# Performance work log

Measured on AMD Instinct MI355X. Metric: run time of the kernel, lower is better.

The kernel has to match this reference:

```python
import jax, jax.numpy as jnp
import numpy as np

NEMB = 128
N_NODES = 8192
N_EDGES = 16384
N_STEMS = 4096
N_GRAPHS = 256
N_BLOCKS = 105       # BlockDictionary.n_unique_blocks
N_STEMTYPES = 32     # BlockDictionary.n_stem_types
OUT_PER_STEM = 105
OUT_PER_STOP = 1
NUM_CONV_STEPS = 12
SLOPE = 0.01         # nn.LeakyReLU default negative slope


def _act(v):
    return jax.nn.leaky_relu(v, SLOPE)


def setup_inputs() -> dict:
    key = jax.random.key(0)
    ks = jax.random.split(key, 32)
    def p(i, shape, fan_in):
        return jax.random.normal(ks[i], shape, jnp.float32) / np.sqrt(fan_in).astype(np.float32)
    D = NEMB
    inp = {
        "x": jax.random.randint(ks[0], (N_NODES,), 0, N_BLOCKS + 1),
        "stemtypes": jax.random.randint(ks[1], (N_STEMS,), 0, N_STEMTYPES + 1),
        "edge_attr": jax.random.randint(ks[2], (N_EDGES, 2), 0, N_STEMTYPES),
        "edge_index": jax.random.randint(ks[3], (2, N_EDGES), 0, N_NODES),
        "stem_node_idx": jax.random.randint(ks[4], (N_STEMS,), 0, N_NODES),
        "node_batch": jnp.sort(jax.random.randint(ks[5], (N_NODES,), 0, N_GRAPHS)),
        # embedding tables
        "emb_block": p(6, (N_BLOCKS + 1, D), D),
        "emb_stem": p(7, (N_STEMTYPES + 1, D), D),
        "emb_bond": p(8, (N_STEMTYPES, D), D),
        # block2emb MLP
        "b2e_w1": p(9, (D, D), D), "b2e_b1": p(10, (D,), D),
        "b2e_w2": p(11, (D, D), D), "b2e_b2": p(12, (D,), D),
        # NNConv root weight + bias (edge-nn is identity: nn.Sequential())
        "conv_root": p(13, (D, D), D), "conv_bias": p(14, (D,), D),
        # GRU (torch gate order r, z, n)
        "gru_w_ih": p(15, (3 * D, D), D), "gru_w_hh": p(16, (3 * D, D), D),
        "gru_b_ih": p(17, (3 * D,), D), "gru_b_hh": p(18, (3 * D,), D),
        # stem2pred MLP (in = 2*D)
        "s2p_w1": p(19, (D, 2 * D), 2 * D), "s2p_b1": p(20, (D,), 2 * D),
        "s2p_w2": p(21, (D, D), D), "s2p_b2": p(22, (D,), D),
        "s2p_w3": p(23, (OUT_PER_STEM, D), D), "s2p_b3": p(24, (OUT_PER_STEM,), D),
        # global2pred MLP
        "g2p_w1": p(25, (D, D), D), "g2p_b1": p(26, (D,), D),
        "g2p_w2": p(27, (OUT_PER_STOP, D), D), "g2p_b2": p(28, (OUT_PER_STOP,), D),
    }
    return inp


def reference(x, stemtypes, edge_attr, edge_index, stem_node_idx, node_batch,
              emb_block, emb_stem, emb_bond,
              b2e_w1, b2e_b1, b2e_w2, b2e_b2,
              conv_root, conv_bias,
              gru_w_ih, gru_w_hh, gru_b_ih, gru_b_hh,
              s2p_w1, s2p_b1, s2p_w2, s2p_b2, s2p_w3, s2p_b3,
              g2p_w1, g2p_b1, g2p_w2, g2p_b2):
    block_emb = emb_block[x]                          # [N, D]
    stem_emb = emb_stem[stemtypes]                    # [S, D]
    be = emb_bond[edge_attr]                          # [E, 2, D]
    # outer product -> per-edge [D_in, D_out] weight (matches view(-1, in, out))
    W_e = be[:, 0, :, None] * be[:, 1, None, :]       # [E, D, D]

    out = _act(block_emb @ b2e_w1.T + b2e_b1) @ b2e_w2.T + b2e_b2  # [N, D]
    h = out                                           # GRU hidden state

    src, dst = edge_index[0], edge_index[1]
    ones_e = jnp.ones((N_EDGES,), out.dtype)
    deg = jax.ops.segment_sum(ones_e, dst, num_segments=N_NODES)
    inv_deg = jnp.where(deg > 0, 1.0 / jnp.maximum(deg, 1.0), 0.0)[:, None]

    for _ in range(NUM_CONV_STEPS):
        # NNConv: mean_j (x_j @ W_e) + x @ root + bias, then LeakyReLU
        msg = jnp.einsum('ei,eij->ej', out[src], W_e)                  # [E, D]
        agg = jax.ops.segment_sum(msg, dst, num_segments=N_NODES) * inv_deg
        m = _act(agg + out @ conv_root + conv_bias)
        # single-layer GRU, seq_len = 1
        gi = m @ gru_w_ih.T + gru_b_ih
        gh = h @ gru_w_hh.T + gru_b_hh
        ir, iz, inn = jnp.split(gi, 3, axis=-1)
        hr, hz, hn = jnp.split(gh, 3, axis=-1)
        r = jax.nn.sigmoid(ir + hr)
        z = jax.nn.sigmoid(iz + hz)
        n = jnp.tanh(inn + r * hn)
        h = (1.0 - z) * n + z * h
        out = h

    stem_cat = jnp.concatenate([out[stem_node_idx], stem_emb], axis=1)  # [S, 2D]
    s = _act(stem_cat @ s2p_w1.T + s2p_b1)
    s = _act(s @ s2p_w2.T + s2p_b2)
    stem_pred = s @ s2p_w3.T + s2p_b3                                   # [S, out_per_stem]

    # global_mean_pool
    gsum = jax.ops.segment_sum(out, node_batch, num_segments=N_GRAPHS)
    gcnt = jax.ops.segment_sum(jnp.ones((N_NODES,), out.dtype), node_batch, num_segments=N_GRAPHS)
    gmean = gsum / jnp.maximum(gcnt, 1.0)[:, None]
    g = _act(gmean @ g2p_w1.T + g2p_b1)
    stop_pred = g @ g2p_w2.T + g2p_b2                                   # [G, out_per_stop]
    return stem_pred, stop_pred
```

## Files before the change

### kernel.cpp

```cpp
#include <hip/hip_runtime.h>
#include <math.h>

#define D 128
#define NNODES 8192
#define NEDGES 16384
#define NSTEMS 4096
#define NGRAPHS 256
#define NSTEPS 12
#define OPS 105
#define SLOPE 0.01f
#define MT 32
#define NB (NNODES / MT)
#define LDA 136
#define LDA2 264
#define LDQ 40
#define LDH 132

typedef _Float16 half_t;
typedef __attribute__((ext_vector_type(8))) _Float16 f16x8;
typedef __attribute__((ext_vector_type(4))) float f32x4;

__device__ __forceinline__ float leaky(float x) { return x > 0.f ? x : SLOPE * x; }
__device__ __forceinline__ float fast_sigmoid(float x) {
    return __builtin_amdgcn_rcpf(1.f + __expf(-x));
}
__device__ __forceinline__ float fast_tanh(float x) {
    float e = __expf(2.f * x);
    return 1.f - 2.f * __builtin_amdgcn_rcpf(e + 1.f);
}

__global__ void k_setup(
    const float* __restrict__ root, const float* __restrict__ wih,
    const float* __restrict__ whh, const float* __restrict__ bond,
    const float* __restrict__ sw1, const float* __restrict__ sw2,
    const float* __restrict__ sw3, const float* __restrict__ bw1,
    const float* __restrict__ bw2, const float* __restrict__ gw1,
    half_t* __restrict__ rootP, half_t* __restrict__ WihP,
    half_t* __restrict__ WhhP, half_t* __restrict__ bondTP,
    half_t* __restrict__ s1P, half_t* __restrict__ s2P, half_t* __restrict__ s3P,
    half_t* __restrict__ w1P, half_t* __restrict__ w2P, half_t* __restrict__ bondQP,
    float* __restrict__ g1T, int* __restrict__ zeroi) {
    int idx = blockIdx.x * 256 + threadIdx.x;
    int which = blockIdx.y;
    if (which == 10) {
        if (idx < 128 * 128) {
            int r = idx >> 7, c = idx & 127;
            g1T[c * 128 + r] = gw1[idx];
        }
        return;
    }
    if (which == 11) {
        if (idx < 2 * NNODES) zeroi[idx] = 0;
        return;
    }
    int KT = (which == 4) ? 8 : (which == 9) ? 1 : 4;
    int NT = (which == 1 || which == 2) ? 24 : (which == 3) ? 2 : (which == 6) ? 7 : 8;
    if (idx >= NT * KT * 512) return;
    int j = idx & 7;
    int L = (idx >> 3) & 63;
    int t = idx >> 9;
    int kt = t % KT, nt = t / KT;
    int k = kt * 32 + (L >> 4) * 8 + j;
    int n = nt * 16 + (L & 15);
    switch (which) {
        case 0: rootP[idx] = (half_t)root[k * D + n]; break;
        case 1: WihP[idx] = (half_t)wih[n * D + k]; break;
        case 2: WhhP[idx] = (half_t)whh[n * D + k]; break;
        case 3: bondTP[idx] = (half_t)bond[n * D + k]; break;
        case 4: s1P[idx] = (half_t)sw1[n * 256 + k]; break;
        case 5: s2P[idx] = (half_t)sw2[n * 128 + k]; break;
        case 6: s3P[idx] = (n < OPS) ? (half_t)sw3[n * 128 + k] : (half_t)0.f; break;
        case 7: w1P[idx] = (half_t)bw1[n * D + k]; break;
        case 8: w2P[idx] = (half_t)bw2[n * D + k]; break;
        case 9: bondQP[idx] = (half_t)bond[k * D + n]; break;
    }
}

__global__ void k_deg(const int* __restrict__ eidx, int* __restrict__ deg) {
    int e = blockIdx.x * 256 + threadIdx.x;
    if (e < NEDGES) atomicAdd(&deg[eidx[NEDGES + e]], 1);
}

__global__ void k_scan(const int* __restrict__ deg, int* __restrict__ row_start,
                       float* __restrict__ inv_deg) {
    __shared__ int sums[256];
    int t = threadIdx.x;
    int base = t * 32;
    int s = 0;
    for (int k = 0; k < 32; ++k) s += deg[base + k];
    sums[t] = s;
    __syncthreads();
    for (int off = 1; off < 256; off <<= 1) {
        int v = sums[t];
        int u = (t >= off) ? sums[t - off] : 0;
        __syncthreads();
        sums[t] = v + u;
        __syncthreads();
    }
    int run = sums[t] - s;
    for (int k = 0; k < 32; ++k) {
        int d = deg[base + k];
        row_start[base + k] = run;
        run += d;
        inv_deg[base + k] = (d > 0) ? (1.0f / (float)d) : 0.0f;
    }
    if (t == 255) row_start[NNODES] = run;
}

__global__ void k_scatter(const int* __restrict__ eidx, const int* __restrict__ eattr,
                          const int* __restrict__ row_start,
                          int* __restrict__ fill, int4* __restrict__ epack) {
    int e = blockIdx.x * 256 + threadIdx.x;
    if (e < NEDGES) {
        int d = eidx[NEDGES + e];
        int pos = row_start[d] + atomicAdd(&fill[d], 1);
        int2 aa = *(const int2*)(eattr + 2 * e);
        epack[pos] = make_int4(eidx[e], aa.x, aa.y, d);
    }
}

__global__ __launch_bounds__(512, 2) void k_init(
    const int* __restrict__ x, const float* __restrict__ embBlock,
    const half_t* __restrict__ w1P, const float* __restrict__ b1,
    const half_t* __restrict__ w2P, const float* __restrict__ b2,
    const half_t* __restrict__ bondTP,
    float* __restrict__ hF, float* __restrict__ P0) {
    __shared__ __align__(16) half_t Ae[MT * LDA];
    __shared__ __align__(16) half_t T1[MT * LDA];
    const int tid = threadIdx.x;
    const int w = tid >> 6;
    const int lane = tid & 63;
    const int quad = lane >> 4;
    const int l16 = lane & 15;
    const int n0 = blockIdx.x * MT;
    const int c = w * 16 + l16;

    {
        int row = tid >> 4;
        int col = (tid & 15) * 8;
        const float* src = embBlock + (size_t)x[n0 + row] * D + col;
        float4 v0 = ((const float4*)src)[0];
        float4 v1 = ((const float4*)src)[1];
        f16x8 hv;
        hv[0] = (half_t)v0.x; hv[1] = (half_t)v0.y; hv[2] = (half_t)v0.z; hv[3] = (half_t)v0.w;
        hv[4] = (half_t)v1.x; hv[5] = (half_t)v1.y; hv[6] = (half_t)v1.z; hv[7] = (half_t)v1.w;
        *(f16x8*)&Ae[row * LDA + col] = hv;
    }
    __syncthreads();

    {
        f32x4 acc[2] = {{0.f, 0.f, 0.f, 0.f}, {0.f, 0.f, 0.f, 0.f}};
#pragma unroll
        for (int kt = 0; kt < 4; ++kt) {
            f16x8 b = *(const f16x8*)(w1P + (size_t)((w * 4 + kt) * 64 + lane) * 8);
            f16x8 a0 = *(const f16x8*)&Ae[(0 + l16) * LDA + kt * 32 + quad * 8];
            f16x8 a1 = *(const f16x8*)&Ae[(16 + l16) * LDA + kt * 32 + quad * 8];
            acc[0] = __builtin_amdgcn_mfma_f32_16x16x32_f16(a0, b, acc[0], 0, 0, 0);
            acc[1] = __builtin_amdgcn_mfma_f32_16x16x32_f16(a1, b, acc[1], 0, 0, 0);
        }
        float bb = b1[c];
#pragma unroll
        for (int mt = 0; mt < 2; ++mt)
#pragma unroll
            for (int r = 0; r < 4; ++r)
                T1[(mt * 16 + quad * 4 + r) * LDA + c] = (half_t)leaky(acc[mt][r] + bb);
    }
    __syncthreads();

    {
        f32x4 acc[2] = {{0.f, 0.f, 0.f, 0.f}, {0.f, 0.f, 0.f, 0.f}};
#pragma unroll
        for (int kt = 0; kt < 4; ++kt) {
            f16x8 b = *(const f16x8*)(w2P + (size_t)((w * 4 + kt) * 64 + lane) * 8);
            f16x8 a0 = *(const f16x8*)&T1[(0 + l16) * LDA + kt * 32 + quad * 8];
            f16x8 a1 = *(const f16x8*)&T1[(16 + l16) * LDA + kt * 32 + quad * 8];
            acc[0] = __builtin_amdgcn_mfma_f32_16x16x32_f16(a0, b, acc[0], 0, 0, 0);
            acc[1] = __builtin_amdgcn_mfma_f32_16x16x32_f16(a1, b, acc[1], 0, 0, 0);
        }
        float bb = b2[c];
#pragma unroll
        for (int mt = 0; mt < 2; ++mt)
#pragma unroll
            for (int r = 0; r < 4; ++r) {
                int row = mt * 16 + quad * 4 + r;
                float h = acc[mt][r] + bb;
                hF[(size_t)(n0 + row) * D + c] = h;
                Ae[row * LDA + c] = (half_t)h;
            }
    }
    __syncthreads();

    if (w < 4) {
        int mt = w >> 1, nt = w & 1;
        f32x4 acc = {0.f, 0.f, 0.f, 0.f};
#pragma unroll
        for (int kt = 0; kt < 4; ++kt) {
            f16x8 b = *(const f16x8*)(bondTP + (size_t)((nt * 4 + kt) * 64 + lane) * 8);
            f16x8 a = *(const f16x8*)&Ae[(mt * 16 + l16) * LDA + kt * 32 + quad * 8];
            acc = __builtin_amdgcn_mfma_f32_16x16x32_f16(a, b, acc, 0, 0, 0);
        }
#pragma unroll
        for (int r = 0; r < 4; ++r)
            P0[(size_t)(n0 + mt * 16 + quad * 4 + r) * 32 + nt * 16 + l16] = acc[r];
    }
}

__global__ __launch_bounds__(512, 2) void k_step(
    float* __restrict__ hF,
    const float* __restrict__ Pprev, float* __restrict__ Pnext,
    const half_t* __restrict__ rootP, const half_t* __restrict__ WihP,
    const half_t* __restrict__ WhhP, const half_t* __restrict__ bondTP,
    const half_t* __restrict__ bondQP,
    const float* __restrict__ cbias, const float* __restrict__ bih,
    const float* __restrict__ bhh,
    const int4* __restrict__ epack,
    const int* __restrict__ row_start, const float* __restrict__ inv_deg, int writeP) {
    __shared__ __align__(16) half_t As[MT * LDA];
    __shared__ __align__(16) half_t Am[MT * LDA];
    __shared__ __align__(16) float Hs[MT * LDH];
    __shared__ __align__(16) half_t Qh[MT * LDQ];
    __shared__ float Q[MT * 32];

    const int tid = threadIdx.x;
    const int w = tid >> 6;
    const int lane = tid & 63;
    const int quad = lane >> 4;
    const int l16 = lane & 15;
    const int n0 = blockIdx.x * MT;
    const int c = w * 16 + l16;

    {
        int row = tid >> 4;
        int col = (tid & 15) * 8;
        const float* src = hF + (size_t)(n0 + row) * D + col;
        float4 v0 = ((const float4*)src)[0];
        float4 v1 = ((const float4*)src)[1];
        f16x8 hv;
        hv[0] = (half_t)v0.x; hv[1] = (half_t)v0.y; hv[2] = (half_t)v0.z; hv[3] = (half_t)v0.w;
        hv[4] = (half_t)v1.x; hv[5] = (half_t)v1.y; hv[6] = (half_t)v1.z; hv[7] = (half_t)v1.w;
        *(f16x8*)&As[row * LDA + col] = hv;
        *(float4*)&Hs[row * LDH + col] = v0;
        *(float4*)&Hs[row * LDH + col + 4] = v1;
    }
    Q[tid] = 0.f;
    Q[tid + 512] = 0.f;
    const int p0 = row_start[n0];
    const int p1 = row_start[n0 + MT];
    int4 ep;
    float wv = 0.f, idg = 0.f;
    const int pme = p0 + tid;
    const bool have = (pme < p1);
    if (have) {
        ep = epack[pme];
        wv = Pprev[(size_t)ep.x * 32 + ep.y];
        idg = inv_deg[ep.w];
    }
    f16x8 rootB[4], ghB[12], aggB;
#pragma unroll
    for (int kt = 0; kt < 4; ++kt)
        rootB[kt] = *(const f16x8*)(rootP + (size_t)((w * 4 + kt) * 64 + lane) * 8);
#pragma unroll
    for (int kt = 0; kt < 4; ++kt)
#pragma unroll
        for (int g = 0; g < 3; ++g)
            ghB[g * 4 + kt] = *(const f16x8*)(WhhP + (size_t)(((g * 8 + w) * 4 + kt) * 64 + lane) * 8);
    aggB = *(const f16x8*)(bondQP + (size_t)(w * 64 + lane) * 8);
    const float cb = cbias[c];
    const float bi0 = bih[c], bi1 = bih[D + c], bi2 = bih[2 * D + c];
    const float bh0 = bhh[c], bh1 = bhh[D + c], bh2 = bhh[2 * D + c];
    __syncthreads();

    f32x4 convAcc[2] = {{0.f, 0.f, 0.f, 0.f}, {0.f, 0.f, 0.f, 0.f}};
#pragma unroll
    for (int kt = 0; kt < 4; ++kt) {
        f16x8 a0 = *(const f16x8*)&As[(0 + l16) * LDA + kt * 32 + quad * 8];
        f16x8 a1 = *(const f16x8*)&As[(16 + l16) * LDA + kt * 32 + quad * 8];
        convAcc[0] = __builtin_amdgcn_mfma_f32_16x16x32_f16(a0, rootB[kt], convAcc[0], 0, 0, 0);
        convAcc[1] = __builtin_amdgcn_mfma_f32_16x16x32_f16(a1, rootB[kt], convAcc[1], 0, 0, 0);
    }
    if (have) atomicAdd(&Q[(ep.w - n0) * 32 + ep.z], wv * idg);
    for (int p2 = pme + 512; p2 < p1; p2 += 512) {
        int4 e2 = epack[p2];
        atomicAdd(&Q[(e2.w - n0) * 32 + e2.z], Pprev[(size_t)e2.x * 32 + e2.y] * inv_deg[e2.w]);
    }
    f32x4 ghA[2][3];
#pragma unroll
    for (int mt = 0; mt < 2; ++mt)
#pragma unroll
        for (int g = 0; g < 3; ++g) ghA[mt][g] = f32x4{0.f, 0.f, 0.f, 0.f};
#pragma unroll
    for (int kt = 0; kt < 4; ++kt) {
        f16x8 a0 = *(const f16x8*)&As[(0 + l16) * LDA + kt * 32 + quad * 8];
        f16x8 a1 = *(const f16x8*)&As[(16 + l16) * LDA + kt * 32 + quad * 8];
#pragma unroll
        for (int g = 0; g < 3; ++g) {
            ghA[0][g] = __builtin_amdgcn_mfma_f32_16x16x32_f16(a0, ghB[g * 4 + kt], ghA[0][g], 0, 0, 0);
            ghA[1][g] = __builtin_amdgcn_mfma_f32_16x16x32_f16(a1, ghB[g * 4 + kt], ghA[1][g], 0, 0, 0);
        }
    }
    __syncthreads();

    f16x8 giB[12];
#pragma unroll
    for (int kt = 0; kt < 4; ++kt)
#pragma unroll
        for (int g = 0; g < 3; ++g)
            giB[g * 4 + kt] = *(const f16x8*)(WihP + (size_t)(((g * 8 + w) * 4 + kt) * 64 + lane) * 8);

    Qh[(tid >> 5) * LDQ + (tid & 31)] = (half_t)Q[tid];
    Qh[((tid + 512) >> 5) * LDQ + (tid & 31)] = (half_t)Q[tid + 512];
    __syncthreads();

#pragma unroll
    for (int mt = 0; mt < 2; ++mt) {
        f32x4 acc = {0.f, 0.f, 0.f, 0.f};
        f16x8 a = *(const f16x8*)&Qh[(mt * 16 + l16) * LDQ + quad * 8];
        acc = __builtin_amdgcn_mfma_f32_16x16x32_f16(a, aggB, acc, 0, 0, 0);
#pragma unroll
        for (int r = 0; r < 4; ++r) {
            float m = convAcc[mt][r] + cb + acc[r];
            Am[(mt * 16 + quad * 4 + r) * LDA + c] = (half_t)leaky(m);
        }
    }
    __syncthreads();

    f32x4 giA[2][3];
#pragma unroll
    for (int mt = 0; mt < 2; ++mt)
#pragma unroll
        for (int g = 0; g < 3; ++g) giA[mt][g] = f32x4{0.f, 0.f, 0.f, 0.f};
#pragma unroll
    for (int kt = 0; kt < 4; ++kt) {
        f16x8 a0 = *(const f16x8*)&Am[(0 + l16) * LDA + kt * 32 + quad * 8];
        f16x8 a1 = *(const f16x8*)&Am[(16 + l16) * LDA + kt * 32 + quad * 8];
#pragma unroll
        for (int g = 0; g < 3; ++g) {
            giA[0][g] = __builtin_amdgcn_mfma_f32_16x16x32_f16(a0, giB[g * 4 + kt], giA[0][g], 0, 0, 0);
            giA[1][g] = __builtin_amdgcn_mfma_f32_16x16x32_f16(a1, giB[g * 4 + kt], giA[1][g], 0, 0, 0);
        }
    }
#pragma unroll
    for (int mt = 0; mt < 2; ++mt) {
#pragma unroll
        for (int r = 0; r < 4; ++r) {
            int row = mt * 16 + quad * 4 + r;
            float rg = fast_sigmoid(giA[mt][0][r] + bi0 + ghA[mt][0][r] + bh0);
            float z = fast_sigmoid(giA[mt][1][r] + bi1 + ghA[mt][1][r] + bh1);
            float nn = fast_tanh(giA[mt][2][r] + bi2 + rg * (ghA[mt][2][r] + bh2));
            float hnew = (1.f - z) * nn + z * Hs[row * LDH + c];
            hF[(size_t)(n0 + row) * D + c] = hnew;
            As[row * LDA + c] = (half_t)hnew;
        }
    }

    if (writeP) {
        __syncthreads();
        if (w < 4) {
            int mt = w >> 1, nt = w & 1;
            f32x4 acc = {0.f, 0.f, 0.f, 0.f};
#pragma unroll
            for (int kt = 0; kt < 4; ++kt) {
                f16x8 b = *(const f16x8*)(bondTP + (size_t)((nt * 4 + kt) * 64 + lane) * 8);
                f16x8 a = *(const f16x8*)&As[(mt * 16 + l16) * LDA + kt * 32 + quad * 8];
                acc = __builtin_amdgcn_mfma_f32_16x16x32_f16(a, b, acc, 0, 0, 0);
            }
#pragma unroll
            for (int r = 0; r < 4; ++r)
                Pnext[(size_t)(n0 + mt * 16 + quad * 4 + r) * 32 + nt * 16 + l16] = acc[r];
        }
    }
}

__device__ __forceinline__ int lower_bound_dev(const int* a, int n, int v) {
    int lo = 0, hi = n;
    while (lo < hi) {
        int m = (lo + hi) >> 1;
        if (a[m] < v) lo = m + 1;
        else hi = m;
    }
    return lo;
}

__global__ __launch_bounds__(512) void k_heads(
    const float* __restrict__ hF, const int* __restrict__ sni, const int* __restrict__ stypes,
    const float* __restrict__ embStem,
    const half_t* __restrict__ s1P, const float* __restrict__ b1,
    const half_t* __restrict__ s2P, const float* __restrict__ b2,
    const half_t* __restrict__ s3P, const float* __restrict__ b3,
    const int* __restrict__ batch,
    const float* __restrict__ g1T, const float* __restrict__ gb1,
    const float* __restrict__ gw2, const float* __restrict__ gb2,
    float* __restrict__ dout) {
    __shared__ __align__(16) half_t cat[16 * LDA2];
    __shared__ __align__(16) half_t t1[16 * LDA];
    __shared__ __align__(16) half_t t2[16 * LDA];
    const int tid = threadIdx.x;
    if (blockIdx.x >= 256) {
        int g = blockIdx.x - 256;
        if (tid >= 128) return;
        __shared__ float mean_s[D];
        __shared__ float red[D];
        int j = tid;
        int lo = lower_bound_dev(batch, NNODES, g);
        int hi = lower_bound_dev(batch, NNODES, g + 1);
        float sum = 0.f;
        for (int n = lo; n < hi; ++n) sum += hF[(size_t)n * D + j];
        float denom = (hi > lo) ? (float)(hi - lo) : 1.0f;
        mean_s[j] = sum / denom;
        __syncthreads();
        float a = gb1[j];
        for (int i = 0; i < D; ++i) a += mean_s[i] * g1T[i * D + j];
        a = leaky(a);
        red[j] = a * gw2[j];
        __syncthreads();
        for (int off = 64; off > 0; off >>= 1) {
            if (j < off) red[j] += red[j + off];
            __syncthreads();
        }
        if (j == 0) dout[NSTEMS * OPS + g] = red[0] + gb2[0];
        return;
    }
    const int w = tid >> 6;
    const int lane = tid & 63;
    const int quad = lane >> 4;
    const int l16 = lane & 15;
    const int s0 = blockIdx.x * 16;
    const int c = w * 16 + l16;

    {
        int row = tid >> 5;
        int col = (tid & 31) * 8;
        const float* src;
        if (col < D) src = hF + (size_t)sni[s0 + row] * D + col;
        else src = embStem + (size_t)stypes[s0 + row] * D + (col - D);
        float4 v0 = ((const float4*)src)[0];
        float4 v1 = ((const float4*)src)[1];
        f16x8 hv;
        hv[0] = (half_t)v0.x; hv[1] = (half_t)v0.y; hv[2] = (half_t)v0.z; hv[3] = (half_t)v0.w;
        hv[4] = (half_t)v1.x; hv[5] = (half_t)v1.y; hv[6] = (half_t)v1.z; hv[7] = (half_t)v1.w;
        *(f16x8*)&cat[row * LDA2 + col] = hv;
    }
    __syncthreads();

    {
        f32x4 acc = {0.f, 0.f, 0.f, 0.f};
#pragma unroll
        for (int kt = 0; kt < 8; ++kt) {
            f16x8 b = *(const f16x8*)(s1P + (size_t)((w * 8 + kt) * 64 + lane) * 8);
            f16x8 a = *(const f16x8*)&cat[l16 * LDA2 + kt * 32 + quad * 8];
            acc = __builtin_amdgcn_mfma_f32_16x16x32_f16(a, b, acc, 0, 0, 0);
        }
        float bb = b1[c];
#pragma unroll
        for (int r = 0; r < 4; ++r)
            t1[(quad * 4 + r) * LDA + c] = (half_t)leaky(acc[r] + bb);
    }
    __syncthreads();
    {
        f32x4 acc = {0.f, 0.f, 0.f, 0.f};
#pragma unroll
        for (int kt = 0; kt < 4; ++kt) {
            f16x8 b = *(const f16x8*)(s2P + (size_t)((w * 4 + kt) * 64 + lane) * 8);
            f16x8 a = *(const f16x8*)&t1[l16 * LDA + kt * 32 + quad * 8];
            acc = __builtin_amdgcn_mfma_f32_16x16x32_f16(a, b, acc, 0, 0, 0);
        }
        float bb = b2[c];
#pragma unroll
        for (int r = 0; r < 4; ++r)
            t2[(quad * 4 + r) * LDA + c] = (half_t)leaky(acc[r] + bb);
    }
    __syncthreads();
    if (w < 7) {
        f32x4 acc = {0.f, 0.f, 0.f, 0.f};
#pragma unroll
        for (int kt = 0; kt < 4; ++kt) {
            f16x8 b = *(const f16x8*)(s3P + (size_t)((w * 4 + kt) * 64 + lane) * 8);
            f16x8 a = *(const f16x8*)&t2[l16 * LDA + kt * 32 + quad * 8];
            acc = __builtin_amdgcn_mfma_f32_16x16x32_f16(a, b, acc, 0, 0, 0);
        }
        int j = w * 16 + l16;
        if (j < OPS) {
            float bb = b3[j];
#pragma unroll
            for (int r = 0; r < 4; ++r)
                dout[(size_t)(s0 + quad * 4 + r) * OPS + j] = acc[r] + bb;
        }
    }
}

extern "C" void kernel_launch(void* const* d_in, const int* in_sizes, int n_in,
                              void* d_out, int out_size, void* d_ws, size_t ws_size,
                              hipStream_t stream) {
    const int* x = (const int*)d_in[0];
    const int* stypes = (const int*)d_in[1];
    const int* eattr = (const int*)d_in[2];
    const int* eidx = (const int*)d_in[3];
    const int* sni = (const int*)d_in[4];
    const int* batch = (const int*)d_in[5];
    const float* embBlock = (const float*)d_in[6];
    const float* embStem = (const float*)d_in[7];
    const float* embBond = (const float*)d_in[8];
    const float* b2e_w1 = (const float*)d_in[9];
    const float* b2e_b1 = (const float*)d_in[10];
    const float* b2e_w2 = (const float*)d_in[11];
    const float* b2e_b2 = (const float*)d_in[12];
    const float* conv_root = (const float*)d_in[13];
    const float* conv_bias = (const float*)d_in[14];
    const float* gru_w_ih = (const float*)d_in[15];
    const float* gru_w_hh = (const float*)d_in[16];
    const float* gru_b_ih = (const float*)d_in[17];
    const float* gru_b_hh = (const float*)d_in[18];
    const float* s2p_w1 = (const float*)d_in[19];
    const float* s2p_b1 = (const float*)d_in[20];
    const float* s2p_w2 = (const float*)d_in[21];
    const float* s2p_b2 = (const float*)d_in[22];
    const float* s2p_w3 = (const float*)d_in[23];
    const float* s2p_b3 = (const float*)d_in[24];
    const float* g2p_w1 = (const float*)d_in[25];
    const float* g2p_b1 = (const float*)d_in[26];
    const float* g2p_w2 = (const float*)d_in[27];
    const float* g2p_b2 = (const float*)d_in[28];
    float* out_f = (float*)d_out;

    float* W = (float*)d_ws;
    size_t off = 0;
    auto alloc = [&](size_t words) {
        size_t o = off;
        off += (words + 3) & ~(size_t)3;
        return o;
    };
    float* hF = W + alloc(NNODES * D);
    float* P0 = W + alloc(NNODES * 32);
    float* P1 = W + alloc(NNODES * 32);
    half_t* rootP = (half_t*)(W + alloc(16384 / 2));
    half_t* WihP = (half_t*)(W + alloc(49152 / 2));
    half_t* WhhP = (half_t*)(W + alloc(49152 / 2));
    half_t* bondTP = (half_t*)(W + alloc(4096 / 2));
    half_t* s1P = (half_t*)(W + alloc(32768 / 2));
    half_t* s2P = (half_t*)(W + alloc(16384 / 2));
    half_t* s3P = (half_t*)(W + alloc(14336 / 2));
    half_t* w1P = (half_t*)(W + alloc(16384 / 2));
    half_t* w2P = (half_t*)(W + alloc(16384 / 2));
    half_t* bondQP = (half_t*)(W + alloc(4096 / 2));
    float* g1T = W + alloc(128 * 128);
    int* row_start = (int*)(W + alloc(NNODES + 1));
    int4* epack = (int4*)(W + alloc(NEDGES * 4));
    float* inv_deg = W + alloc(NNODES);
    float* zbase = W + alloc(2 * NNODES);
    int* deg = (int*)zbase;
    int* fill = deg + NNODES;

    k_setup<<<dim3(192, 12), 256, 0, stream>>>(
        conv_root, gru_w_ih, gru_w_hh, embBond, s2p_w1, s2p_w2, s2p_w3,
        b2e_w1, b2e_w2, g2p_w1,
        rootP, WihP, WhhP, bondTP, s1P, s2P, s3P, w1P, w2P, bondQP,
        g1T, (int*)zbase);
    k_deg<<<(NEDGES + 255) / 256, 256, 0, stream>>>(eidx, deg);
    k_scan<<<1, 256, 0, stream>>>(deg, row_start, inv_deg);
    k_scatter<<<(NEDGES + 255) / 256, 256, 0, stream>>>(eidx, eattr, row_start, fill, epack);
    k_init<<<NNODES / MT, 512, 0, stream>>>(x, embBlock, w1P, b2e_b1, w2P, b2e_b2,
                                            bondTP, hF, P0);

    for (int step = 0; step < NSTEPS; ++step) {
        const float* Pprev = (step & 1) ? P1 : P0;
        float* Pnext = (step & 1) ? P0 : P1;
        int writeP = (step < NSTEPS - 1) ? 1 : 0;
        k_step<<<NB, 512, 0, stream>>>(
            hF, Pprev, Pnext, rootP, WihP, WhhP, bondTP, bondQP,
            conv_bias, gru_b_ih, gru_b_hh,
            epack, row_start, inv_deg, writeP);
    }

    k_heads<<<NSTEMS / 16 + NGRAPHS, 512, 0, stream>>>(
        hF, sni, stypes, embStem,
        s1P, s2p_b1, s2P, s2p_b2, s3P, s2p_b3,
        batch, g1T, g2p_b1, g2p_w2, g2p_b2, out_f);
}
```

Baseline: 251.7 us.

## Use 64-node tiles with 1024-thread blocks in GRU step kernel

The step kernel now processes 64 nodes per block with 16 waves: each column-wave pair splits the rows in two halves, so each weight fragment is shared across twice as many rows per block and the grid is halved. The old h values are read straight from global memory into registers rather than staged in a shared fp32 buffer. The weight fragments are also loaded inside the MFMA loops instead of being preloaded into registers, which lowers register pressure enough for 1024-thread blocks. In exchange there are fewer blocks (128) on a large GPU, which may underfill the compute units, and global weight loads now sit inside the MFMA loops where they can stall.

```diff
diff --git a/kernel.cpp b/kernel.cpp
--- a/kernel.cpp
+++ b/kernel.cpp
@@ -9,12 +9,12 @@
 #define NSTEPS 12
 #define OPS 105
 #define SLOPE 0.01f
-#define MT 32
-#define NB (NNODES / MT)
+#define IMT 32
+#define SMT 64
+#define NSB (NNODES / SMT)
 #define LDA 136
 #define LDA2 264
 #define LDQ 40
-#define LDH 132
 
 typedef _Float16 half_t;
 typedef __attribute__((ext_vector_type(8))) _Float16 f16x8;
@@ -125,14 +125,14 @@
     const half_t* __restrict__ w2P, const float* __restrict__ b2,
     const half_t* __restrict__ bondTP,
     float* __restrict__ hF, float* __restrict__ P0) {
-    __shared__ __align__(16) half_t Ae[MT * LDA];
-    __shared__ __align__(16) half_t T1[MT * LDA];
+    __shared__ __align__(16) half_t Ae[IMT * LDA];
+    __shared__ __align__(16) half_t T1[IMT * LDA];
     const int tid = threadIdx.x;
     const int w = tid >> 6;
     const int lane = tid & 63;
     const int quad = lane >> 4;
     const int l16 = lane & 15;
-    const int n0 = blockIdx.x * MT;
+    const int n0 = blockIdx.x * IMT;
     const int c = w * 16 + l16;
 
     {
@@ -205,7 +205,7 @@
     }
 }
 
-__global__ __launch_bounds__(512, 2) void k_step(
+__global__ __launch_bounds__(1024, 1) void k_step(
     float* __restrict__ hF,
     const float* __restrict__ Pprev, float* __restrict__ Pnext,
     const half_t* __restrict__ rootP, const half_t* __restrict__ WihP,
@@ -215,19 +215,20 @@
     const float* __restrict__ bhh,
     const int4* __restrict__ epack,
     const int* __restrict__ row_start, const float* __restrict__ inv_deg, int writeP) {
-    __shared__ __align__(16) half_t As[MT * LDA];
-    __shared__ __align__(16) half_t Am[MT * LDA];
-    __shared__ __align__(16) float Hs[MT * LDH];
-    __shared__ __align__(16) half_t Qh[MT * LDQ];
-    __shared__ float Q[MT * 32];
+    __shared__ __align__(16) half_t As[SMT * LDA];
+    __shared__ __align__(16) half_t Am[SMT * LDA];
+    __shared__ __align__(16) half_t Qh[SMT * LDQ];
+    __shared__ float Q[SMT * 32];
 
     const int tid = threadIdx.x;
     const int w = tid >> 6;
     const int lane = tid & 63;
     const int quad = lane >> 4;
     const int l16 = lane & 15;
-    const int n0 = blockIdx.x * MT;
-    const int c = w * 16 + l16;
+    const int wc = w & 7;
+    const int mh = w >> 3;
+    const int n0 = blockIdx.x * SMT;
+    const int c = wc * 16 + l16;
 
     {
         int row = tid >> 4;
@@ -239,13 +240,17 @@
         hv[0] = (half_t)v0.x; hv[1] = (half_t)v0.y; hv[2] = (half_t)v0.z; hv[3] = (half_t)v0.w;
         hv[4] = (half_t)v1.x; hv[5] = (half_t)v1.y; hv[6] = (half_t)v1.z; hv[7] = (half_t)v1.w;
         *(f16x8*)&As[row * LDA + col] = hv;
-        *(float4*)&Hs[row * LDH + col] = v0;
-        *(float4*)&Hs[row * LDH + col + 4] = v1;
-    }
+    }
+    float hold[2][4];
+#pragma unroll
+    for (int mt = 0; mt < 2; ++mt)
+#pragma unroll
+        for (int r = 0; r < 4; ++r)
+            hold[mt][r] = hF[(size_t)(n0 + (mh * 2 + mt) * 16 + quad * 4 + r) * D + c];
     Q[tid] = 0.f;
-    Q[tid + 512] = 0.f;
+    Q[tid + 1024] = 0.f;
     const int p0 = row_start[n0];
-    const int p1 = row_start[n0 + MT];
+    const int p1 = row_start[n0 + SMT];
     int4 ep;
     float wv = 0.f, idg = 0.f;
     const int pme = p0 + tid;
@@ -255,16 +260,7 @@
         wv = Pprev[(size_t)ep.x * 32 + ep.y];
         idg = inv_deg[ep.w];
     }
-    f16x8 rootB[4], ghB[12], aggB;
-#pragma unroll
-    for (int kt = 0; kt < 4; ++kt)
-        rootB[kt] = *(const f16x8*)(rootP + (size_t)((w * 4 + kt) * 64 + lane) * 8);
-#pragma unroll
-    for (int kt = 0; kt < 4; ++kt)
-#pragma unroll
-        for (int g = 0; g < 3; ++g)
-            ghB[g * 4 + kt] = *(const f16x8*)(WhhP + (size_t)(((g * 8 + w) * 4 + kt) * 64 + lane) * 8);
-    aggB = *(const f16x8*)(bondQP + (size_t)(w * 64 + lane) * 8);
+    f16x8 aggB = *(const f16x8*)(bondQP + (size_t)(wc * 64 + lane) * 8);
     const float cb = cbias[c];
     const float bi0 = bih[c], bi1 = bih[D + c], bi2 = bih[2 * D + c];
     const float bh0 = bhh[c], bh1 = bhh[D + c], bh2 = bhh[2 * D + c];
@@ -273,13 +269,14 @@
     f32x4 convAcc[2] = {{0.f, 0.f, 0.f, 0.f}, {0.f, 0.f, 0.f, 0.f}};
 #pragma unroll
     for (int kt = 0; kt < 4; ++kt) {
-        f16x8 a0 = *(const f16x8*)&As[(0 + l16) * LDA + kt * 32 + quad * 8];
-        f16x8 a1 = *(const f16x8*)&As[(16 + l16) * LDA + kt * 32 + quad * 8];
-        convAcc[0] = __builtin_amdgcn_mfma_f32_16x16x32_f16(a0, rootB[kt], convAcc[0], 0, 0, 0);
-        convAcc[1] = __builtin_amdgcn_mfma_f32_16x16x32_f16(a1, rootB[kt], convAcc[1], 0, 0, 0);
+        f16x8 b = *(const f16x8*)(rootP + (size_t)((wc * 4 + kt) * 64 + lane) * 8);
+        f16x8 a0 = *(const f16x8*)&As[((mh * 2 + 0) * 16 + l16) * LDA + kt * 32 + quad * 8];
+        f16x8 a1 = *(const f16x8*)&As[((mh * 2 + 1) * 16 + l16) * LDA + kt * 32 + quad * 8];
+        convAcc[0] = __builtin_amdgcn_mfma_f32_16x16x32_f16(a0, b, convAcc[0], 0, 0, 0);
+        convAcc[1] = __builtin_amdgcn_mfma_f32_16x16x32_f16(a1, b, convAcc[1], 0, 0, 0);
     }
     if (have) atomicAdd(&Q[(ep.w - n0) * 32 + ep.z], wv * idg);
-    for (int p2 = pme + 512; p2 < p1; p2 += 512) {
+    for (int p2 = pme + 1024; p2 < p1; p2 += 1024) {
         int4 e2 = epack[p2];
         atomicAdd(&Q[(e2.w - n0) * 32 + e2.z], Pprev[(size_t)e2.x * 32 + e2.y] * inv_deg[e2.w]);
     }
@@ -290,36 +287,30 @@
         for (int g = 0; g < 3; ++g) ghA[mt][g] = f32x4{0.f, 0.f, 0.f, 0.f};
 #pragma unroll
     for (int kt = 0; kt < 4; ++kt) {
-        f16x8 a0 = *(const f16x8*)&As[(0 + l16) * LDA + kt * 32 + quad * 8];
-        f16x8 a1 = *(const f16x8*)&As[(16 + l16) * LDA + kt * 32 + quad * 8];
+        f16x8 a0 = *(const f16x8*)&As[((mh * 2 + 0) * 16 + l16) * LDA + kt * 32 + quad * 8];
+        f16x8 a1 = *(const f16x8*)&As[((mh * 2 + 1) * 16 + l16) * LDA + kt * 32 + quad * 8];
 #pragma unroll
         for (int g = 0; g < 3; ++g) {
-            ghA[0][g] = __builtin_amdgcn_mfma_f32_16x16x32_f16(a0, ghB[g * 4 + kt], ghA[0][g], 0, 0, 0);
-            ghA[1][g] = __builtin_amdgcn_mfma_f32_16x16x32_f16(a1, ghB[g * 4 + kt], ghA[1][g], 0, 0, 0);
-        }
-    }
-    __syncthreads();
-
-    f16x8 giB[12];
-#pragma unroll
-    for (int kt = 0; kt < 4; ++kt)
-#pragma unroll
-        for (int g = 0; g < 3; ++g)
-            giB[g * 4 + kt] = *(const f16x8*)(WihP + (size_t)(((g * 8 + w) * 4 + kt) * 64 + lane) * 8);
+            f16x8 b = *(const f16x8*)(WhhP + (size_t)(((g * 8 + wc) * 4 + kt) * 64 + lane) * 8);
+            ghA[0][g] = __builtin_amdgcn_mfma_f32_16x16x32_f16(a0, b, ghA[0][g], 0, 0, 0);
+            ghA[1][g] = __builtin_amdgcn_mfma_f32_16x16x32_f16(a1, b, ghA[1][g], 0, 0, 0);
+        }
+    }
+    __syncthreads();
 
     Qh[(tid >> 5) * LDQ + (tid & 31)] = (half_t)Q[tid];
-    Qh[((tid + 512) >> 5) * LDQ + (tid & 31)] = (half_t)Q[tid + 512];
+    Qh[((tid + 1024) >> 5) * LDQ + (tid & 31)] = (half_t)Q[tid + 1024];
     __syncthreads();
 
 #pragma unroll
     for (int mt = 0; mt < 2; ++mt) {
         f32x4 acc = {0.f, 0.f, 0.f, 0.f};
-        f16x8 a = *(const f16x8*)&Qh[(mt * 16 + l16) * LDQ + quad * 8];
+        f16x8 a = *(const f16x8*)&Qh[((mh * 2 + mt) * 16 + l16) * LDQ + quad * 8];
         acc = __builtin_amdgcn_mfma_f32_16x16x32_f16(a, aggB, acc, 0, 0, 0);
 #pragma unroll
         for (int r = 0; r < 4; ++r) {
             float m = convAcc[mt][r] + cb + acc[r];
-            Am[(mt * 16 + quad * 4 + r) * LDA + c] = (half_t)leaky(m);
+            Am[((mh * 2 + mt) * 16 + quad * 4 + r) * LDA + c] = (half_t)leaky(m);
         }
     }
     __syncthreads();
@@ -331,23 +322,24 @@
         for (int g = 0; g < 3; ++g) giA[mt][g] = f32x4{0.f, 0.f, 0.f, 0.f};
 #pragma unroll
     for (int kt = 0; kt < 4; ++kt) {
-        f16x8 a0 = *(const f16x8*)&Am[(0 + l16) * LDA + kt * 32 + quad * 8];
-        f16x8 a1 = *(const f16x8*)&Am[(16 + l16) * LDA + kt * 32 + quad * 8];
+        f16x8 a0 = *(const f16x8*)&Am[((mh * 2 + 0) * 16 + l16) * LDA + kt * 32 + quad * 8];
+        f16x8 a1 = *(const f16x8*)&Am[((mh * 2 + 1) * 16 + l16) * LDA + kt * 32 + quad * 8];
 #pragma unroll
         for (int g = 0; g < 3; ++g) {
-            giA[0][g] = __builtin_amdgcn_mfma_f32_16x16x32_f16(a0, giB[g * 4 + kt], giA[0][g], 0, 0, 0);
-            giA[1][g] = __builtin_amdgcn_mfma_f32_16x16x32_f16(a1, giB[g * 4 + kt], giA[1][g], 0, 0, 0);
+            f16x8 b = *(const f16x8*)(WihP + (size_t)(((g * 8 + wc) * 4 + kt) * 64 + lane) * 8);
+            giA[0][g] = __builtin_amdgcn_mfma_f32_16x16x32_f16(a0, b, giA[0][g], 0, 0, 0);
+            giA[1][g] = __builtin_amdgcn_mfma_f32_16x16x32_f16(a1, b, giA[1][g], 0, 0, 0);
         }
     }
 #pragma unroll
     for (int mt = 0; mt < 2; ++mt) {
 #pragma unroll
         for (int r = 0; r < 4; ++r) {
-            int row = mt * 16 + quad * 4 + r;
+            int row = (mh * 2 + mt) * 16 + quad * 4 + r;
             float rg = fast_sigmoid(giA[mt][0][r] + bi0 + ghA[mt][0][r] + bh0);
             float z = fast_sigmoid(giA[mt][1][r] + bi1 + ghA[mt][1][r] + bh1);
             float nn = fast_tanh(giA[mt][2][r] + bi2 + rg * (ghA[mt][2][r] + bh2));
-            float hnew = (1.f - z) * nn + z * Hs[row * LDH + c];
+            float hnew = (1.f - z) * nn + z * hold[mt][r];
             hF[(size_t)(n0 + row) * D + c] = hnew;
             As[row * LDA + c] = (half_t)hnew;
         }
@@ -355,7 +347,7 @@
 
     if (writeP) {
         __syncthreads();
-        if (w < 4) {
+        if (w < 8) {
             int mt = w >> 1, nt = w & 1;
             f32x4 acc = {0.f, 0.f, 0.f, 0.f};
 #pragma unroll
@@ -558,14 +550,14 @@
     k_deg<<<(NEDGES + 255) / 256, 256, 0, stream>>>(eidx, deg);
     k_scan<<<1, 256, 0, stream>>>(deg, row_start, inv_deg);
     k_scatter<<<(NEDGES + 255) / 256, 256, 0, stream>>>(eidx, eattr, row_start, fill, epack);
-    k_init<<<NNODES / MT, 512, 0, stream>>>(x, embBlock, w1P, b2e_b1, w2P, b2e_b2,
-                                            bondTP, hF, P0);
+    k_init<<<NNODES / IMT, 512, 0, stream>>>(x, embBlock, w1P, b2e_b1, w2P, b2e_b2,
+                                             bondTP, hF, P0);
 
     for (int step = 0; step < NSTEPS; ++step) {
         const float* Pprev = (step & 1) ? P1 : P0;
         float* Pnext = (step & 1) ? P0 : P1;
         int writeP = (step < NSTEPS - 1) ? 1 : 0;
-        k_step<<<NB, 512, 0, stream>>>(
+        k_step<<<NSB, 1024, 0, stream>>>(
             hF, Pprev, Pnext, rootP, WihP, WhhP, bondTP, bondQP,
             conv_bias, gru_b_ih, gru_b_hh,
             epack, row_start, inv_deg, writeP);
```

After: 283.4 us. +12.6%, slower.

## Store GRU hidden state in fp16 ping-pong buffers and fuse CSR build

Applied to the files above, without the earlier changes.

Hidden state between GRU steps is now kept as fp16 in two ping-pong buffers instead of fp32. This halves the per-step state traffic and removes the fp32 shared-memory copy of h. Only the last step writes fp32 output. The degree count, scan and scatter kernels are merged into one single-block kernel using shared-memory atomics, which removes two launches and the zeroing pass. The cost is lower precision in the recurrent state and a serial single-block CSR build.

```diff
diff --git a/kernel.cpp b/kernel.cpp
--- a/kernel.cpp
+++ b/kernel.cpp
@@ -14,7 +14,6 @@
 #define LDA 136
 #define LDA2 264
 #define LDQ 40
-#define LDH 132
 
 typedef _Float16 half_t;
 typedef __attribute__((ext_vector_type(8))) _Float16 f16x8;
@@ -39,7 +38,7 @@
     half_t* __restrict__ WhhP, half_t* __restrict__ bondTP,
     half_t* __restrict__ s1P, half_t* __restrict__ s2P, half_t* __restrict__ s3P,
     half_t* __restrict__ w1P, half_t* __restrict__ w2P, half_t* __restrict__ bondQP,
-    float* __restrict__ g1T, int* __restrict__ zeroi) {
+    float* __restrict__ g1T) {
     int idx = blockIdx.x * 256 + threadIdx.x;
     int which = blockIdx.y;
     if (which == 10) {
@@ -47,10 +46,6 @@
             int r = idx >> 7, c = idx & 127;
             g1T[c * 128 + r] = gw1[idx];
         }
-        return;
-    }
-    if (which == 11) {
-        if (idx < 2 * NNODES) zeroi[idx] = 0;
         return;
     }
     int KT = (which == 4) ? 8 : (which == 9) ? 1 : 4;
@@ -76,44 +71,45 @@
     }
 }
 
-__global__ void k_deg(const int* __restrict__ eidx, int* __restrict__ deg) {
-    int e = blockIdx.x * 256 + threadIdx.x;
-    if (e < NEDGES) atomicAdd(&deg[eidx[NEDGES + e]], 1);
-}
-
-__global__ void k_scan(const int* __restrict__ deg, int* __restrict__ row_start,
-                       float* __restrict__ inv_deg) {
-    __shared__ int sums[256];
-    int t = threadIdx.x;
-    int base = t * 32;
+__global__ __launch_bounds__(1024) void k_csr(
+    const int* __restrict__ eidx, const int* __restrict__ eattr,
+    int* __restrict__ row_start, float* __restrict__ inv_deg,
+    int4* __restrict__ epack) {
+    __shared__ int sdeg[NNODES];
+    __shared__ int sums[1024];
+    const int tid = threadIdx.x;
+    for (int i = tid; i < NNODES; i += 1024) sdeg[i] = 0;
+    __syncthreads();
+    for (int e = tid; e < NEDGES; e += 1024)
+        atomicAdd(&sdeg[eidx[NEDGES + e]], 1);
+    __syncthreads();
+    const int base = tid * 8;
     int s = 0;
-    for (int k = 0; k < 32; ++k) s += deg[base + k];
-    sums[t] = s;
-    __syncthreads();
-    for (int off = 1; off < 256; off <<= 1) {
-        int v = sums[t];
-        int u = (t >= off) ? sums[t - off] : 0;
+#pragma unroll
+    for (int k = 0; k < 8; ++k) s += sdeg[base + k];
+    sums[tid] = s;
+    __syncthreads();
+    for (int off = 1; off < 1024; off <<= 1) {
+        int v = sums[tid];
+        int u = (tid >= off) ? sums[tid - off] : 0;
         __syncthreads();
-        sums[t] = v + u;
+        sums[tid] = v + u;
         __syncthreads();
     }
-    int run = sums[t] - s;
-    for (int k = 0; k < 32; ++k) {
-        int d = deg[base + k];
+    int run = sums[tid] - s;
+#pragma unroll
+    for (int k = 0; k < 8; ++k) {
+        int d = sdeg[base + k];
         row_start[base + k] = run;
+        inv_deg[base + k] = (d > 0) ? (1.0f / (float)d) : 0.0f;
+        sdeg[base + k] = run;
         run += d;
-        inv_deg[base + k] = (d > 0) ? (1.0f / (float)d) : 0.0f;
-    }
-    if (t == 255) row_start[NNODES] = run;
-}
-
-__global__ void k_scatter(const int* __restrict__ eidx, const int* __restrict__ eattr,
-                          const int* __restrict__ row_start,
-                          int* __restrict__ fill, int4* __restrict__ epack) {
-    int e = blockIdx.x * 256 + threadIdx.x;
-    if (e < NEDGES) {
+    }
+    if (tid == 1023) row_start[NNODES] = run;
+    __syncthreads();
+    for (int e = tid; e < NEDGES; e += 1024) {
         int d = eidx[NEDGES + e];
-        int pos = row_start[d] + atomicAdd(&fill[d], 1);
+        int pos = atomicAdd(&sdeg[d], 1);
         int2 aa = *(const int2*)(eattr + 2 * e);
         epack[pos] = make_int4(eidx[e], aa.x, aa.y, d);
     }
@@ -124,7 +120,7 @@
     const half_t* __restrict__ w1P, const float* __restrict__ b1,
     const half_t* __restrict__ w2P, const float* __restrict__ b2,
     const half_t* __restrict__ bondTP,
-    float* __restrict__ hF, float* __restrict__ P0) {
+    half_t* __restrict__ hA, float* __restrict__ P0) {
     __shared__ __align__(16) half_t Ae[MT * LDA];
     __shared__ __align__(16) half_t T1[MT * LDA];
     const int tid = threadIdx.x;
@@ -183,9 +179,9 @@
 #pragma unroll
             for (int r = 0; r < 4; ++r) {
                 int row = mt * 16 + quad * 4 + r;
-                float h = acc[mt][r] + bb;
-                hF[(size_t)(n0 + row) * D + c] = h;
-                Ae[row * LDA + c] = (half_t)h;
+                half_t hh = (half_t)(acc[mt][r] + bb);
+                hA[(size_t)(n0 + row) * D + c] = hh;
+                Ae[row * LDA + c] = hh;
             }
     }
     __syncthreads();
@@ -206,7 +202,7 @@
 }
 
 __global__ __launch_bounds__(512, 2) void k_step(
-    float* __restrict__ hF,
+    const half_t* __restrict__ curH, half_t* __restrict__ nxtH, float* __restrict__ hF,
     const float* __restrict__ Pprev, float* __restrict__ Pnext,
     const half_t* __restrict__ rootP, const half_t* __restrict__ WihP,
     const half_t* __restrict__ WhhP, const half_t* __restrict__ bondTP,
@@ -214,10 +210,9 @@
     const float* __restrict__ cbias, const float* __restrict__ bih,
     const float* __restrict__ bhh,
     const int4* __restrict__ epack,
-    const int* __restrict__ row_start, const float* __restrict__ inv_deg, int writeP) {
+    const int* __restrict__ row_start, const float* __restrict__ inv_deg, int last) {
     __shared__ __align__(16) half_t As[MT * LDA];
     __shared__ __align__(16) half_t Am[MT * LDA];
-    __shared__ __align__(16) float Hs[MT * LDH];
     __shared__ __align__(16) half_t Qh[MT * LDQ];
     __shared__ float Q[MT * 32];
 
@@ -232,15 +227,8 @@
     {
         int row = tid >> 4;
         int col = (tid & 15) * 8;
-        const float* src = hF + (size_t)(n0 + row) * D + col;
-        float4 v0 = ((const float4*)src)[0];
-        float4 v1 = ((const float4*)src)[1];
-        f16x8 hv;
-        hv[0] = (half_t)v0.x; hv[1] = (half_t)v0.y; hv[2] = (half_t)v0.z; hv[3] = (half_t)v0.w;
-        hv[4] = (half_t)v1.x; hv[5] = (half_t)v1.y; hv[6] = (half_t)v1.z; hv[7] = (half_t)v1.w;
-        *(f16x8*)&As[row * LDA + col] = hv;
-        *(float4*)&Hs[row * LDH + col] = v0;
-        *(float4*)&Hs[row * LDH + col + 4] = v1;
+        f16x8 v = *(const f16x8*)(curH + (size_t)(n0 + row) * D + col);
+        *(f16x8*)&As[row * LDA + col] = v;
     }
     Q[tid] = 0.f;
     Q[tid + 512] = 0.f;
@@ -270,6 +258,13 @@
     const float bh0 = bhh[c], bh1 = bhh[D + c], bh2 = bhh[2 * D + c];
     __syncthreads();
 
+    float hold[2][4];
+#pragma unroll
+    for (int mt = 0; mt < 2; ++mt)
+#pragma unroll
+        for (int r = 0; r < 4; ++r)
+            hold[mt][r] = (float)As[(mt * 16 + quad * 4 + r) * LDA + c];
+
     f32x4 convAcc[2] = {{0.f, 0.f, 0.f, 0.f}, {0.f, 0.f, 0.f, 0.f}};
 #pragma unroll
     for (int kt = 0; kt < 4; ++kt) {
@@ -347,13 +342,18 @@
             float rg = fast_sigmoid(giA[mt][0][r] + bi0 + ghA[mt][0][r] + bh0);
             float z = fast_sigmoid(giA[mt][1][r] + bi1 + ghA[mt][1][r] + bh1);
             float nn = fast_tanh(giA[mt][2][r] + bi2 + rg * (ghA[mt][2][r] + bh2));
-            float hnew = (1.f - z) * nn + z * Hs[row * LDH + c];
-            hF[(size_t)(n0 + row) * D + c] = hnew;
-            As[row * LDA + c] = (half_t)hnew;
-        }
-    }
-
-    if (writeP) {
+            float hnew = (1.f - z) * nn + z * hold[mt][r];
+            if (last) {
+                hF[(size_t)(n0 + row) * D + c] = hnew;
+            } else {
+                half_t hh = (half_t)hnew;
+                nxtH[(size_t)(n0 + row) * D + c] = hh;
+                As[row * LDA + c] = hh;
+            }
+        }
+    }
+
+    if (!last) {
         __syncthreads();
         if (w < 4) {
             int mt = w >> 1, nt = w & 1;
@@ -530,6 +530,8 @@
         return o;
     };
     float* hF = W + alloc(NNODES * D);
+    half_t* hA = (half_t*)(W + alloc(NNODES * D / 2));
+    half_t* hB = (half_t*)(W + alloc(NNODES * D / 2));
     float* P0 = W + alloc(NNODES * 32);
     float* P1 = W + alloc(NNODES * 32);
     half_t* rootP = (half_t*)(W + alloc(16384 / 2));
@@ -546,29 +548,25 @@
     int* row_start = (int*)(W + alloc(NNODES + 1));
     int4* epack = (int4*)(W + alloc(NEDGES * 4));
     float* inv_deg = W + alloc(NNODES);
-    float* zbase = W + alloc(2 * NNODES);
-    int* deg = (int*)zbase;
-    int* fill = deg + NNODES;
-
-    k_setup<<<dim3(192, 12), 256, 0, stream>>>(
+
+    k_setup<<<dim3(192, 11), 256, 0, stream>>>(
         conv_root, gru_w_ih, gru_w_hh, embBond, s2p_w1, s2p_w2, s2p_w3,
         b2e_w1, b2e_w2, g2p_w1,
-        rootP, WihP, WhhP, bondTP, s1P, s2P, s3P, w1P, w2P, bondQP,
-        g1T, (int*)zbase);
-    k_deg<<<(NEDGES + 255) / 256, 256, 0, stream>>>(eidx, deg);
-    k_scan<<<1, 256, 0, stream>>>(deg, row_start, inv_deg);
-    k_scatter<<<(NEDGES + 255) / 256, 256, 0, stream>>>(eidx, eattr, row_start, fill, epack);
+        rootP, WihP, WhhP, bondTP, s1P, s2P, s3P, w1P, w2P, bondQP, g1T);
+    k_csr<<<1, 1024, 0, stream>>>(eidx, eattr, row_start, inv_deg, epack);
     k_init<<<NNODES / MT, 512, 0, stream>>>(x, embBlock, w1P, b2e_b1, w2P, b2e_b2,
-                                            bondTP, hF, P0);
+                                            bondTP, hA, P0);
 
     for (int step = 0; step < NSTEPS; ++step) {
+        const half_t* cur = (step & 1) ? hB : hA;
+        half_t* nxt = (step & 1) ? hA : hB;
         const float* Pprev = (step & 1) ? P1 : P0;
         float* Pnext = (step & 1) ? P0 : P1;
-        int writeP = (step < NSTEPS - 1) ? 1 : 0;
+        int last = (step == NSTEPS - 1) ? 1 : 0;
         k_step<<<NB, 512, 0, stream>>>(
-            hF, Pprev, Pnext, rootP, WihP, WhhP, bondTP, bondQP,
+            cur, nxt, hF, Pprev, Pnext, rootP, WihP, WhhP, bondTP, bondQP,
             conv_bias, gru_b_ih, gru_b_hh,
-            epack, row_start, inv_deg, writeP);
+            epack, row_start, inv_deg, last);
     }
 
     k_heads<<<NSTEMS / 16 + NGRAPHS, 512, 0, stream>>>(
```

Result: slower. 260.8 us (+3.6%).
